# Kernel optimization log

Hardware: AMD Instinct MI355X
Metric: run time of the kernel (lower is better)

The kernel has to match this reference:

```python
import jax, jax.numpy as jnp
import numpy as np

B, H, W = 4, 64, 1024
h, w = 32, 512
K = 16
C = 64
EPS = 1e-5


def setup_inputs() -> dict:
    key = jax.random.key(0)
    ks = jax.random.split(key, 8)
    n_sampled = h * w
    xyz_proj = jax.random.normal(ks[0], (B, H, W, 3), dtype=jnp.float32)
    points_proj = jax.random.normal(ks[1], (B, H, W, C), dtype=jnp.float32)
    xyz_sampled_proj = jax.random.normal(ks[2], (B, h, w, 3), dtype=jnp.float32)
    # Precomputed neighbor selection (stand-in for fused_conv_random_k, which is
    # a non-differentiable custom CUDA op producing detached indices + mask).
    neighbor_idx = jax.random.randint(ks[3], (B, n_sampled * K), 0, H * W, dtype=jnp.int32)
    valid_mask = (jax.random.uniform(ks[4], (B, n_sampled, K, 1)) > 0.1).astype(jnp.float32)
    # 1x1 conv MLP params (torch Conv2d weight (out,in,1,1) stored here as (in,out))
    def mk(k, cin, cout):
        kw, = jax.random.split(k, 1)
        wgt = jax.random.normal(kw, (cin, cout), dtype=jnp.float32) * (1.0 / np.sqrt(cin))
        return wgt
    w0 = mk(ks[5], 3 + C, 64)
    w1 = mk(ks[6], 64, 64)
    w2 = mk(ks[7], 64, 128)
    z = lambda c: jnp.zeros((c,), jnp.float32)
    o = lambda c: jnp.ones((c,), jnp.float32)
    return dict(
        xyz_proj=xyz_proj, points_proj=points_proj, xyz_sampled_proj=xyz_sampled_proj,
        neighbor_idx=neighbor_idx, valid_mask=valid_mask,
        w0=w0, b0=z(64), g0=o(64), be0=z(64), m0=z(64), v0=o(64),
        w1=w1, b1=z(64), g1=o(64), be1=z(64), m1=z(64), v1=o(64),
        w2=w2, b2=z(128), g2=o(128), be2=z(128), m2=z(128), v2=o(128),
    )


def _conv_bn_relu(x, wgt, b, g, be, m, v):
    # 1x1 conv == matmul over channel dim; BN in eval mode with running stats.
    y = jnp.einsum('bnkc,co->bnko', x, wgt) + b
    y = g * (y - m) * jax.lax.rsqrt(v + EPS) + be
    return jax.nn.relu(y)


def reference(xyz_proj, points_proj, xyz_sampled_proj, neighbor_idx, valid_mask,
              w0, b0, g0, be0, m0, v0,
              w1, b1, g1, be1, m1, v1,
              w2, b2, g2, be2, m2, v2):
    Bc = xyz_proj.shape[0]
    Cc = points_proj.shape[3]
    hh, ww = xyz_sampled_proj.shape[1], xyz_sampled_proj.shape[2]
    n_sampled = hh * ww
    xyz_bn3 = xyz_proj.reshape(Bc, -1, 3)          # (B, H*W, 3)
    points_bnc = points_proj.reshape(Bc, -1, Cc)   # (B, H*W, C)
    idx = neighbor_idx[..., None]                  # (B, n*K, 1)
    new_xyz_group = jnp.take_along_axis(xyz_bn3, idx, axis=1).reshape(Bc, n_sampled, K, 3)
    new_points_group = jnp.take_along_axis(points_bnc, idx, axis=1).reshape(Bc, n_sampled, K, Cc)
    new_xyz_group = new_xyz_group * valid_mask
    new_points_group = new_points_group * valid_mask
    new_xyz = xyz_sampled_proj.reshape(Bc, n_sampled, 1, 3)
    xyz_diff = new_xyz_group - new_xyz             # broadcast over K
    feat = jnp.concatenate([xyz_diff, new_points_group], axis=-1)  # (B, n, K, 3+C)
    feat = _conv_bn_relu(feat, w0, b0, g0, be0, m0, v0)
    feat = _conv_bn_relu(feat, w1, b1, g1, be1, m1, v1)
    feat = _conv_bn_relu(feat, w2, b2, g2, be2, m2, v2)
    points_down_sample = jnp.max(feat, axis=2)     # (B, n, 128) max-pool over K
    points_down_sample_proj = points_down_sample.reshape(Bc, hh, ww, -1)
    return points_down_sample, points_down_sample_proj
```

## Files before the change

### kernel.cpp

```cpp
#include <hip/hip_runtime.h>


#define NGRP_    8192
#define OUTHALF_ 8388608
#define WS_      72
#define XS2_     36
#define EPS_     1e-5f
#define GRID_    768

typedef _Float16 h8    __attribute__((ext_vector_type(8)));
typedef float    f32x4 __attribute__((ext_vector_type(4)));
typedef unsigned u32x2 __attribute__((ext_vector_type(2)));

#define PK(lo, hi) ({                                                          \
    const _Float16 _l = (_Float16)fmaxf((lo), 0.f);                            \
    const _Float16 _h = (_Float16)fmaxf((hi), 0.f);                            \
    (unsigned)__builtin_bit_cast(unsigned short, _l) |                         \
    ((unsigned)__builtin_bit_cast(unsigned short, _h) << 16); })

__global__ __launch_bounds__(256, 3) void pnsa_main(
    const float* __restrict__ xyz,
    const float* __restrict__ pts,
    const float* __restrict__ xyzs,
    const int*   __restrict__ nidx,
    const float* __restrict__ vmask,
    const float* __restrict__ w0, const float* __restrict__ b0,
    const float* __restrict__ g0, const float* __restrict__ be0,
    const float* __restrict__ m0, const float* __restrict__ v0,
    const float* __restrict__ w1, const float* __restrict__ b1,
    const float* __restrict__ g1, const float* __restrict__ be1,
    const float* __restrict__ m1, const float* __restrict__ v1,
    const float* __restrict__ w2, const float* __restrict__ b2,
    const float* __restrict__ g2, const float* __restrict__ be2,
    const float* __restrict__ m2, const float* __restrict__ v2,
    float*       __restrict__ out)
{
    __shared__ __align__(16) _Float16 ldsW1[64 * WS_];
    __shared__ __align__(16) _Float16 ldsW2[128 * WS_];
    __shared__ __align__(16) float    s1sh[64], t1sh[64];
    __shared__ __align__(16) float    s2sh[128], t2sh[128];
    __shared__ __align__(16) unsigned ldsX[4][2][16 * XS2_];

    const int tid  = threadIdx.x;
    const int wave = tid >> 6;
    const int lane = tid & 63;
    const int l15  = lane & 15;
    const int quad = lane >> 4;

    unsigned* XA = &ldsX[wave][0][0];
    unsigned* XB = &ldsX[wave][1][0];

    if (tid < 64) {
        const float s = g1[tid] * rsqrtf(v1[tid] + EPS_);
        s1sh[tid] = s;
        t1sh[tid] = (b1[tid] - m1[tid]) * s + be1[tid];
    }
    if (tid < 128) {
        const float s = g2[tid] * rsqrtf(v2[tid] + EPS_);
        s2sh[tid] = s;
        t2sh[tid] = (b2[tid] - m2[tid]) * s + be2[tid];
    }
    __syncthreads();
    for (int idx = tid; idx < 64 * 64; idx += 256) {
        const int k = idx >> 6, n = idx & 63;
        ldsW1[n * WS_ + k] = (_Float16)(w1[idx] * s1sh[n]);
    }
    for (int idx = tid; idx < 64 * 128; idx += 256) {
        const int k = idx >> 7, n = idx & 127;
        ldsW2[n * WS_ + k] = (_Float16)(w2[idx] * s2sh[n]);
    }
    __syncthreads();

    h8 b0f[4][3];
#pragma unroll
    for (int nt = 0; nt < 4; ++nt) {
        const int ch = nt * 16 + l15;
        const float s = g0[ch] * rsqrtf(v0[ch] + EPS_);
        const float t0 = (b0[ch] - m0[ch]) * s + be0[ch];
#pragma unroll
        for (int kk = 0; kk < 3; ++kk) {
            h8 f;
#pragma unroll
            for (int j = 0; j < 8; ++j) {
                const int k = kk * 32 + quad * 8 + j;
                float wv = 0.f;
                if (k < 64)       wv = w0[(3 + k) * 64 + ch] * s;
                else if (k < 67)  wv = w0[(k - 64) * 64 + ch] * s;
                else if (k == 67) wv = t0;
                f[j] = (_Float16)wv;
            }
            b0f[nt][kk] = f;
        }
    }

    const int g0i = blockIdx.x;
    const int pA0 = (g0i << 3) + (wave << 1);
    int nbA = nidx[(pA0 << 4) + l15];
    int nbB = nidx[((pA0 + 1) << 4) + l15];

    for (int grp = g0i; grp < NGRP_; grp += GRID_) {
        const int pA = (grp << 3) + (wave << 1);
        const int pB = pA + 1;
        const int gn = (grp + GRID_ < NGRP_) ? grp + GRID_ : grp;
        const int pAn = (gn << 3) + (wave << 1);

        const size_t rowA = (size_t)(((pA >> 14) << 16) + nbA);
        const size_t rowB = (size_t)(((pB >> 14) << 16) + nbB);
        h8 qA0, qA1, qB0, qB1;
        {
            const float* pwA = pts + (rowA << 6);
            const float* pwB = pts + (rowB << 6);
            f32x4 r0, r1, r2, r3;
            r0 = *(const f32x4*)(pwA + quad * 8);      r1 = *(const f32x4*)(pwA + quad * 8 + 4);
            r2 = *(const f32x4*)(pwA + 32 + quad * 8); r3 = *(const f32x4*)(pwA + 32 + quad * 8 + 4);
#pragma unroll
            for (int j = 0; j < 4; ++j) { qA0[j]=(_Float16)r0[j]; qA0[4+j]=(_Float16)r1[j];
                                          qA1[j]=(_Float16)r2[j]; qA1[4+j]=(_Float16)r3[j]; }
            r0 = *(const f32x4*)(pwB + quad * 8);      r1 = *(const f32x4*)(pwB + quad * 8 + 4);
            r2 = *(const f32x4*)(pwB + 32 + quad * 8); r3 = *(const f32x4*)(pwB + 32 + quad * 8 + 4);
#pragma unroll
            for (int j = 0; j < 4; ++j) { qB0[j]=(_Float16)r0[j]; qB0[4+j]=(_Float16)r1[j];
                                          qB1[j]=(_Float16)r2[j]; qB1[4+j]=(_Float16)r3[j]; }
        }
        const float mkA = vmask[(pA << 4) + l15];
        const float mkB = vmask[(pB << 4) + l15];
        const float* xgA = xyz + rowA * 3;
        const float* xgB = xyz + rowB * 3;
        const float xgA0 = xgA[0], xgA1 = xgA[1], xgA2 = xgA[2];
        const float xgB0 = xgB[0], xgB1 = xgB[1], xgB2 = xgB[2];
        const float* xsA = xyzs + (size_t)pA * 3;
        const float* xsB = xyzs + (size_t)pB * 3;
        const float xsA0 = xsA[0], xsA1 = xsA[1], xsA2 = xsA[2];
        const float xsB0 = xsB[0], xsB1 = xsB[1], xsB2 = xsB[2];

        const int nbAn = nidx[(pAn << 4) + l15];
        const int nbBn = nidx[((pAn + 1) << 4) + l15];

        if (mkA == 0.0f) { qA0 = (h8)(_Float16)0.f; qA1 = (h8)(_Float16)0.f; }
        if (mkB == 0.0f) { qB0 = (h8)(_Float16)0.f; qB1 = (h8)(_Float16)0.f; }
        h8 aA2 = (h8)(_Float16)0.f, aB2 = (h8)(_Float16)0.f;
        if (quad == 0) {
            aA2[0] = (_Float16)(xgA0 * mkA - xsA0);
            aA2[1] = (_Float16)(xgA1 * mkA - xsA1);
            aA2[2] = (_Float16)(xgA2 * mkA - xsA2);
            aA2[3] = (_Float16)1.0f;
            aB2[0] = (_Float16)(xgB0 * mkB - xsB0);
            aB2[1] = (_Float16)(xgB1 * mkB - xsB1);
            aB2[2] = (_Float16)(xgB2 * mkB - xsB2);
            aB2[3] = (_Float16)1.0f;
        }

#pragma unroll
        for (int nt = 0; nt < 4; ++nt) {
            f32x4 aA = {0.f,0.f,0.f,0.f}, aB = {0.f,0.f,0.f,0.f};
            aA = __builtin_amdgcn_mfma_f32_16x16x32_f16(b0f[nt][0], qA0, aA, 0, 0, 0);
            aA = __builtin_amdgcn_mfma_f32_16x16x32_f16(b0f[nt][1], qA1, aA, 0, 0, 0);
            aA = __builtin_amdgcn_mfma_f32_16x16x32_f16(b0f[nt][2], aA2, aA, 0, 0, 0);
            aB = __builtin_amdgcn_mfma_f32_16x16x32_f16(b0f[nt][0], qB0, aB, 0, 0, 0);
            aB = __builtin_amdgcn_mfma_f32_16x16x32_f16(b0f[nt][1], qB1, aB, 0, 0, 0);
            aB = __builtin_amdgcn_mfma_f32_16x16x32_f16(b0f[nt][2], aB2, aB, 0, 0, 0);
            u32x2 pkA = {PK(aA[0], aA[1]), PK(aA[2], aA[3])};
            u32x2 pkB = {PK(aB[0], aB[1]), PK(aB[2], aB[3])};
            *(u32x2*)(XA + l15 * XS2_ + nt * 8 + quad * 2) = pkA;
            *(u32x2*)(XB + l15 * XS2_ + nt * 8 + quad * 2) = pkB;
        }

        h8 xA0 = *(const h8*)(XA + l15 * XS2_ + quad * 4);
        h8 xA1 = *(const h8*)(XA + l15 * XS2_ + 16 + quad * 4);
        h8 xB0 = *(const h8*)(XB + l15 * XS2_ + quad * 4);
        h8 xB1 = *(const h8*)(XB + l15 * XS2_ + 16 + quad * 4);
#pragma unroll 2
        for (int nt = 0; nt < 4; ++nt) {
            const _Float16* wrow = ldsW1 + (nt * 16 + l15) * WS_ + quad * 8;
            h8 wa = *(const h8*)(wrow);
            h8 wb = *(const h8*)(wrow + 32);
            const f32x4 t1 = *(const f32x4*)(t1sh + nt * 16 + quad * 4);
            f32x4 aA = t1, aB = t1;
            aA = __builtin_amdgcn_mfma_f32_16x16x32_f16(wa, xA0, aA, 0, 0, 0);
            aA = __builtin_amdgcn_mfma_f32_16x16x32_f16(wb, xA1, aA, 0, 0, 0);
            aB = __builtin_amdgcn_mfma_f32_16x16x32_f16(wa, xB0, aB, 0, 0, 0);
            aB = __builtin_amdgcn_mfma_f32_16x16x32_f16(wb, xB1, aB, 0, 0, 0);
            u32x2 pkA = {PK(aA[0], aA[1]), PK(aA[2], aA[3])};
            u32x2 pkB = {PK(aB[0], aB[1]), PK(aB[2], aB[3])};
            *(u32x2*)(XA + l15 * XS2_ + nt * 8 + quad * 2) = pkA;
            *(u32x2*)(XB + l15 * XS2_ + nt * 8 + quad * 2) = pkB;
        }

        h8 yA0 = *(const h8*)(XA + l15 * XS2_ + quad * 4);
        h8 yA1 = *(const h8*)(XA + l15 * XS2_ + 16 + quad * 4);
        h8 yB0 = *(const h8*)(XB + l15 * XS2_ + quad * 4);
        h8 yB1 = *(const h8*)(XB + l15 * XS2_ + 16 + quad * 4);
        float sAlo = 0.f, sAhi = 0.f, sBlo = 0.f, sBhi = 0.f;
#pragma unroll 2
        for (int nt = 0; nt < 8; ++nt) {
            const _Float16* wrow = ldsW2 + (nt * 16 + l15) * WS_ + quad * 8;
            h8 wa = *(const h8*)(wrow);
            h8 wb = *(const h8*)(wrow + 32);
            const float t2 = t2sh[nt * 16 + l15];
            f32x4 aA = {0.f,0.f,0.f,0.f}, aB = {0.f,0.f,0.f,0.f};
            aA = __builtin_amdgcn_mfma_f32_16x16x32_f16(yA0, wa, aA, 0, 0, 0);
            aA = __builtin_amdgcn_mfma_f32_16x16x32_f16(yA1, wb, aA, 0, 0, 0);
            aB = __builtin_amdgcn_mfma_f32_16x16x32_f16(yB0, wa, aB, 0, 0, 0);
            aB = __builtin_amdgcn_mfma_f32_16x16x32_f16(yB1, wb, aB, 0, 0, 0);
            float vA = fmaxf(fmaxf(aA[0], aA[1]), fmaxf(aA[2], aA[3])) + t2;
            float vB = fmaxf(fmaxf(aB[0], aB[1]), fmaxf(aB[2], aB[3])) + t2;
            vA = fmaxf(vA, 0.f);  vB = fmaxf(vB, 0.f);
            vA = fmaxf(vA, __shfl_xor(vA, 16, 64));
            vA = fmaxf(vA, __shfl_xor(vA, 32, 64));
            vB = fmaxf(vB, __shfl_xor(vB, 16, 64));
            vB = fmaxf(vB, __shfl_xor(vB, 32, 64));
            if (nt < 4) {
                sAlo = (quad == nt) ? vA : sAlo;
                sBlo = (quad == nt) ? vB : sBlo;
            } else {
                sAhi = (quad == nt - 4) ? vA : sAhi;
                sBhi = (quad == nt - 4) ? vB : sBhi;
            }
        }
        {
            float* obA = out + ((size_t)pA << 7);
            float* obB = out + ((size_t)pB << 7);
            obA[lane]                  = sAlo;
            obA[64 + lane]             = sAhi;
            obA[OUTHALF_ + lane]       = sAlo;
            obA[OUTHALF_ + 64 + lane]  = sAhi;
            obB[lane]                  = sBlo;
            obB[64 + lane]             = sBhi;
            obB[OUTHALF_ + lane]       = sBlo;
            obB[OUTHALF_ + 64 + lane]  = sBhi;
        }

        nbA = nbAn; nbB = nbBn;
    }
}

extern "C" void kernel_launch(void* const* d_in, const int* in_sizes, int n_in,
                              void* d_out, int out_size, void* d_ws, size_t ws_size,
                              hipStream_t stream) {
    const float* xyz   = (const float*)d_in[0];
    const float* pts   = (const float*)d_in[1];
    const float* xyzs  = (const float*)d_in[2];
    const int*   nidx  = (const int*)d_in[3];
    const float* vmask = (const float*)d_in[4];
    const float *w0 = (const float*)d_in[5],  *b0 = (const float*)d_in[6],
                *g0 = (const float*)d_in[7],  *be0 = (const float*)d_in[8],
                *m0 = (const float*)d_in[9],  *v0 = (const float*)d_in[10];
    const float *w1 = (const float*)d_in[11], *b1 = (const float*)d_in[12],
                *g1 = (const float*)d_in[13], *be1 = (const float*)d_in[14],
                *m1 = (const float*)d_in[15], *v1 = (const float*)d_in[16];
    const float *w2 = (const float*)d_in[17], *b2 = (const float*)d_in[18],
                *g2 = (const float*)d_in[19], *be2 = (const float*)d_in[20],
                *m2 = (const float*)d_in[21], *v2 = (const float*)d_in[22];
    float* outp = (float*)d_out;

    pnsa_main<<<dim3(GRID_), dim3(256), 0, stream>>>(
        xyz, pts, xyzs, nidx, vmask,
        w0, b0, g0, be0, m0, v0,
        w1, b1, g1, be1, m1, v1,
        w2, b2, g2, be2, m2, v2, outp);
}
```

Before: 212.9 us.

## Swizzle LDS layouts, keep BN shifts in registers, raise occupancy and grid

Replaces the padded LDS strides for the weights and activations with XOR-swizzled unpadded layouts, which shrinks shared memory while aiming to avoid bank conflicts. The per-channel BN shift values move from LDS into registers, and the layer-2 bias and ReLU are applied once after the K max-reduction instead of inside every tile, a rewrite that holds because max commutes with a shared per-channel add. Packing now uses the cvt_pkrtz intrinsic, which rounds toward zero instead of to nearest. Launch bounds rise to 4 blocks per SM and the persistent grid to 1024, which may add register pressure.

```diff
diff --git a/kernel.cpp b/kernel.cpp
--- a/kernel.cpp
+++ b/kernel.cpp
@@ -3,22 +3,17 @@
 
 #define NGRP_    8192
 #define OUTHALF_ 8388608
-#define WS_      72
-#define XS2_     36
 #define EPS_     1e-5f
-#define GRID_    768
+#define GRID_    1024
 
 typedef _Float16 h8    __attribute__((ext_vector_type(8)));
 typedef float    f32x4 __attribute__((ext_vector_type(4)));
 typedef unsigned u32x2 __attribute__((ext_vector_type(2)));
 
-#define PK(lo, hi) ({                                                          \
-    const _Float16 _l = (_Float16)fmaxf((lo), 0.f);                            \
-    const _Float16 _h = (_Float16)fmaxf((hi), 0.f);                            \
-    (unsigned)__builtin_bit_cast(unsigned short, _l) |                         \
-    ((unsigned)__builtin_bit_cast(unsigned short, _h) << 16); })
-
-__global__ __launch_bounds__(256, 3) void pnsa_main(
+#define PK2(lo, hi) __builtin_bit_cast(unsigned,                               \
+    __builtin_amdgcn_cvt_pkrtz(fmaxf((lo), 0.f), fmaxf((hi), 0.f)))
+
+__global__ __launch_bounds__(256, 4) void pnsa_main(
     const float* __restrict__ xyz,
     const float* __restrict__ pts,
     const float* __restrict__ xyzs,
@@ -35,41 +30,57 @@
     const float* __restrict__ m2, const float* __restrict__ v2,
     float*       __restrict__ out)
 {
-    __shared__ __align__(16) _Float16 ldsW1[64 * WS_];
-    __shared__ __align__(16) _Float16 ldsW2[128 * WS_];
-    __shared__ __align__(16) float    s1sh[64], t1sh[64];
-    __shared__ __align__(16) float    s2sh[128], t2sh[128];
-    __shared__ __align__(16) unsigned ldsX[4][2][16 * XS2_];
+    __shared__ __align__(16) _Float16 ldsW1[64 * 64];
+    __shared__ __align__(16) _Float16 ldsW2[128 * 64];
+    __shared__ __align__(16) unsigned ldsX[4][2][16 * 32];
 
     const int tid  = threadIdx.x;
     const int wave = tid >> 6;
     const int lane = tid & 63;
     const int l15  = lane & 15;
     const int quad = lane >> 4;
+    const int m    = (l15 & 7) << 2;
+    const int c0   = (quad * 4) ^ m;
+    const int c1   = (16 + quad * 4) ^ m;
 
     unsigned* XA = &ldsX[wave][0][0];
     unsigned* XB = &ldsX[wave][1][0];
 
-    if (tid < 64) {
-        const float s = g1[tid] * rsqrtf(v1[tid] + EPS_);
-        s1sh[tid] = s;
-        t1sh[tid] = (b1[tid] - m1[tid]) * s + be1[tid];
-    }
-    if (tid < 128) {
-        const float s = g2[tid] * rsqrtf(v2[tid] + EPS_);
-        s2sh[tid] = s;
-        t2sh[tid] = (b2[tid] - m2[tid]) * s + be2[tid];
-    }
-    __syncthreads();
     for (int idx = tid; idx < 64 * 64; idx += 256) {
         const int k = idx >> 6, n = idx & 63;
-        ldsW1[n * WS_ + k] = (_Float16)(w1[idx] * s1sh[n]);
+        const float s = g1[n] * rsqrtf(v1[n] + EPS_);
+        const int c = (k >> 1) ^ ((n & 7) << 2);
+        ldsW1[n * 64 + (c << 1) + (k & 1)] = (_Float16)(w1[idx] * s);
     }
     for (int idx = tid; idx < 64 * 128; idx += 256) {
         const int k = idx >> 7, n = idx & 127;
-        ldsW2[n * WS_ + k] = (_Float16)(w2[idx] * s2sh[n]);
-    }
-    __syncthreads();
+        const float s = g2[n] * rsqrtf(v2[n] + EPS_);
+        const int c = (k >> 1) ^ ((n & 7) << 2);
+        ldsW2[n * 64 + (c << 1) + (k & 1)] = (_Float16)(w2[idx] * s);
+    }
+
+    f32x4 t1v[4];
+#pragma unroll
+    for (int nt = 0; nt < 4; ++nt) {
+        const int ch = nt * 16 + quad * 4;
+        const f32x4 gv  = *(const f32x4*)(g1 + ch);
+        const f32x4 vv  = *(const f32x4*)(v1 + ch);
+        const f32x4 bv  = *(const f32x4*)(b1 + ch);
+        const f32x4 mv  = *(const f32x4*)(m1 + ch);
+        const f32x4 bev = *(const f32x4*)(be1 + ch);
+#pragma unroll
+        for (int r = 0; r < 4; ++r) {
+            const float s = gv[r] * rsqrtf(vv[r] + EPS_);
+            t1v[nt][r] = (bv[r] - mv[r]) * s + bev[r];
+        }
+    }
+    float t2lo, t2hi;
+    {
+        const float sa = g2[lane] * rsqrtf(v2[lane] + EPS_);
+        t2lo = (b2[lane] - m2[lane]) * sa + be2[lane];
+        const float sb = g2[64 + lane] * rsqrtf(v2[64 + lane] + EPS_);
+        t2hi = (b2[64 + lane] - m2[64 + lane]) * sb + be2[64 + lane];
+    }
 
     h8 b0f[4][3];
 #pragma unroll
@@ -92,6 +103,7 @@
             b0f[nt][kk] = f;
         }
     }
+    __syncthreads();
 
     const int g0i = blockIdx.x;
     const int pA0 = (g0i << 3) + (wave << 1);
@@ -159,52 +171,51 @@
             aB = __builtin_amdgcn_mfma_f32_16x16x32_f16(b0f[nt][0], qB0, aB, 0, 0, 0);
             aB = __builtin_amdgcn_mfma_f32_16x16x32_f16(b0f[nt][1], qB1, aB, 0, 0, 0);
             aB = __builtin_amdgcn_mfma_f32_16x16x32_f16(b0f[nt][2], aB2, aB, 0, 0, 0);
-            u32x2 pkA = {PK(aA[0], aA[1]), PK(aA[2], aA[3])};
-            u32x2 pkB = {PK(aB[0], aB[1]), PK(aB[2], aB[3])};
-            *(u32x2*)(XA + l15 * XS2_ + nt * 8 + quad * 2) = pkA;
-            *(u32x2*)(XB + l15 * XS2_ + nt * 8 + quad * 2) = pkB;
-        }
-
-        h8 xA0 = *(const h8*)(XA + l15 * XS2_ + quad * 4);
-        h8 xA1 = *(const h8*)(XA + l15 * XS2_ + 16 + quad * 4);
-        h8 xB0 = *(const h8*)(XB + l15 * XS2_ + quad * 4);
-        h8 xB1 = *(const h8*)(XB + l15 * XS2_ + 16 + quad * 4);
+            u32x2 pkA = {PK2(aA[0], aA[1]), PK2(aA[2], aA[3])};
+            u32x2 pkB = {PK2(aB[0], aB[1]), PK2(aB[2], aB[3])};
+            const int cw = (nt * 8 + quad * 2) ^ m;
+            *(u32x2*)(XA + l15 * 32 + cw) = pkA;
+            *(u32x2*)(XB + l15 * 32 + cw) = pkB;
+        }
+
+        h8 xA0 = *(const h8*)(XA + l15 * 32 + c0);
+        h8 xA1 = *(const h8*)(XA + l15 * 32 + c1);
+        h8 xB0 = *(const h8*)(XB + l15 * 32 + c0);
+        h8 xB1 = *(const h8*)(XB + l15 * 32 + c1);
 #pragma unroll 2
         for (int nt = 0; nt < 4; ++nt) {
-            const _Float16* wrow = ldsW1 + (nt * 16 + l15) * WS_ + quad * 8;
-            h8 wa = *(const h8*)(wrow);
-            h8 wb = *(const h8*)(wrow + 32);
-            const f32x4 t1 = *(const f32x4*)(t1sh + nt * 16 + quad * 4);
-            f32x4 aA = t1, aB = t1;
+            const _Float16* wrow = ldsW1 + (nt * 16 + l15) * 64;
+            h8 wa = *(const h8*)(wrow + (c0 << 1));
+            h8 wb = *(const h8*)(wrow + (c1 << 1));
+            f32x4 aA = t1v[nt], aB = t1v[nt];
             aA = __builtin_amdgcn_mfma_f32_16x16x32_f16(wa, xA0, aA, 0, 0, 0);
             aA = __builtin_amdgcn_mfma_f32_16x16x32_f16(wb, xA1, aA, 0, 0, 0);
             aB = __builtin_amdgcn_mfma_f32_16x16x32_f16(wa, xB0, aB, 0, 0, 0);
             aB = __builtin_amdgcn_mfma_f32_16x16x32_f16(wb, xB1, aB, 0, 0, 0);
-            u32x2 pkA = {PK(aA[0], aA[1]), PK(aA[2], aA[3])};
-            u32x2 pkB = {PK(aB[0], aB[1]), PK(aB[2], aB[3])};
-            *(u32x2*)(XA + l15 * XS2_ + nt * 8 + quad * 2) = pkA;
-            *(u32x2*)(XB + l15 * XS2_ + nt * 8 + quad * 2) = pkB;
-        }
-
-        h8 yA0 = *(const h8*)(XA + l15 * XS2_ + quad * 4);
-        h8 yA1 = *(const h8*)(XA + l15 * XS2_ + 16 + quad * 4);
-        h8 yB0 = *(const h8*)(XB + l15 * XS2_ + quad * 4);
-        h8 yB1 = *(const h8*)(XB + l15 * XS2_ + 16 + quad * 4);
+            u32x2 pkA = {PK2(aA[0], aA[1]), PK2(aA[2], aA[3])};
+            u32x2 pkB = {PK2(aB[0], aB[1]), PK2(aB[2], aB[3])};
+            const int cw = (nt * 8 + quad * 2) ^ m;
+            *(u32x2*)(XA + l15 * 32 + cw) = pkA;
+            *(u32x2*)(XB + l15 * 32 + cw) = pkB;
+        }
+
+        h8 yA0 = *(const h8*)(XA + l15 * 32 + c0);
+        h8 yA1 = *(const h8*)(XA + l15 * 32 + c1);
+        h8 yB0 = *(const h8*)(XB + l15 * 32 + c0);
+        h8 yB1 = *(const h8*)(XB + l15 * 32 + c1);
         float sAlo = 0.f, sAhi = 0.f, sBlo = 0.f, sBhi = 0.f;
 #pragma unroll 2
         for (int nt = 0; nt < 8; ++nt) {
-            const _Float16* wrow = ldsW2 + (nt * 16 + l15) * WS_ + quad * 8;
-            h8 wa = *(const h8*)(wrow);
-            h8 wb = *(const h8*)(wrow + 32);
-            const float t2 = t2sh[nt * 16 + l15];
+            const _Float16* wrow = ldsW2 + (nt * 16 + l15) * 64;
+            h8 wa = *(const h8*)(wrow + (c0 << 1));
+            h8 wb = *(const h8*)(wrow + (c1 << 1));
             f32x4 aA = {0.f,0.f,0.f,0.f}, aB = {0.f,0.f,0.f,0.f};
             aA = __builtin_amdgcn_mfma_f32_16x16x32_f16(yA0, wa, aA, 0, 0, 0);
             aA = __builtin_amdgcn_mfma_f32_16x16x32_f16(yA1, wb, aA, 0, 0, 0);
             aB = __builtin_amdgcn_mfma_f32_16x16x32_f16(yB0, wa, aB, 0, 0, 0);
             aB = __builtin_amdgcn_mfma_f32_16x16x32_f16(yB1, wb, aB, 0, 0, 0);
-            float vA = fmaxf(fmaxf(aA[0], aA[1]), fmaxf(aA[2], aA[3])) + t2;
-            float vB = fmaxf(fmaxf(aB[0], aB[1]), fmaxf(aB[2], aB[3])) + t2;
-            vA = fmaxf(vA, 0.f);  vB = fmaxf(vB, 0.f);
+            float vA = fmaxf(fmaxf(aA[0], aA[1]), fmaxf(aA[2], aA[3]));
+            float vB = fmaxf(fmaxf(aB[0], aB[1]), fmaxf(aB[2], aB[3]));
             vA = fmaxf(vA, __shfl_xor(vA, 16, 64));
             vA = fmaxf(vA, __shfl_xor(vA, 32, 64));
             vB = fmaxf(vB, __shfl_xor(vB, 16, 64));
@@ -217,6 +228,8 @@
                 sBhi = (quad == nt - 4) ? vB : sBhi;
             }
         }
+        sAlo = fmaxf(sAlo + t2lo, 0.f);  sAhi = fmaxf(sAhi + t2hi, 0.f);
+        sBlo = fmaxf(sBlo + t2lo, 0.f);  sBhi = fmaxf(sBhi + t2hi, 0.f);
         {
             float* obA = out + ((size_t)pA << 7);
             float* obB = out + ((size_t)pB << 7);
```

Result: slower. 289.4 us (+36.0%).
